# Kernel optimization log

Hardware: AMD Instinct MI355X
Metric: run time of the kernel (lower is better)

## Reference

```python
import jax, jax.numpy as jnp
import numpy as np

N_NODES = 50000
N_EDGES = 320000
D_IN = 256
D_OUT = 256


def setup_inputs() -> dict:
    key = jax.random.key(0)
    k1, k2, k3, k4, k5, k6, k7 = jax.random.split(key, 7)
    s = 1.0 / np.sqrt(D_IN)
    return {
        "node_features": jax.random.normal(k1, (N_NODES, D_IN), dtype=jnp.float32),
        "edge_index": jax.random.randint(k2, (2, N_EDGES), 0, N_NODES, dtype=jnp.int64),
        "w1": jax.random.uniform(k3, (D_OUT, D_IN), jnp.float32, -s, s),
        "w2": jax.random.uniform(k4, (D_OUT, D_IN), jnp.float32, -s, s),
        "w3": jax.random.uniform(k5, (D_OUT, D_IN), jnp.float32, -s, s),
        "b3": jax.random.uniform(k6, (D_OUT,), jnp.float32, -s, s),
    }


def reference(node_features, edge_index, w1, w2, w3, b3):
    # GraphSAGE-style conv: project, gather messages from senders,
    # scatter-sum at receivers, project, combine with self term.
    n = node_features.shape[0]
    proj = node_features @ w3.T + b3                 # [N, D_OUT]
    msgs = proj[edge_index[0]]                       # [E, D_OUT] gather senders
    agg = jax.ops.segment_sum(msgs, edge_index[1], num_segments=n)  # [N, D_OUT]
    out = node_features @ w1.T + agg @ w2.T          # [N, D_OUT]
    return out
```

## Files before the change

kernel.cpp:

```cpp
#include <hip/hip_runtime.h>

#define NN 50000
#define NPAD 50048
#define NE 320000
#define D 256
#define CAP 64

typedef __bf16 bf16x8 __attribute__((ext_vector_type(8)));
typedef float f32x4 __attribute__((ext_vector_type(4)));

__device__ __forceinline__ unsigned short f2bf(float f) {
    unsigned u = __builtin_bit_cast(unsigned, f);
    unsigned r = u + 0x7FFFu + ((u >> 16) & 1u);
    return (unsigned short)(r >> 16);
}
__device__ __forceinline__ float bf2f(unsigned short h) {
    return __builtin_bit_cast(float, (unsigned)h << 16);
}

__global__ __launch_bounds__(256) void prep_weights(
        const float* __restrict__ w1, const float* __restrict__ w2,
        const float* __restrict__ w3, const float* __restrict__ b3,
        unsigned short* __restrict__ WTT, float* __restrict__ bvec) {
    const int j = blockIdx.x;
    const int k = threadIdx.x;
    __shared__ float w2row[D];
    __shared__ float red[D];
    w2row[k] = w2[j * D + k];
    __syncthreads();
    float acc = 0.f;
    #pragma unroll 8
    for (int o = 0; o < D; ++o) acc += w2row[o] * w3[o * D + k];
    WTT[(size_t)j * 512 + k]       = f2bf(w1[j * D + k]);
    WTT[(size_t)j * 512 + D + k]   = f2bf(acc);
    red[k] = w2row[k] * b3[k];
    __syncthreads();
    for (int s = 128; s > 0; s >>= 1) {
        if (k < s) red[k] += red[k + s];
        __syncthreads();
    }
    if (k == 0) bvec[j] = red[0];
}

__global__ __launch_bounds__(256) void convert_x(
        const float* __restrict__ x, unsigned short* __restrict__ xbf) {
    const size_t i = ((size_t)blockIdx.x * 256 + threadIdx.x) * 8;
    if (i >= (size_t)NN * D) return;
    const float4 a = *reinterpret_cast<const float4*>(x + i);
    const float4 b = *reinterpret_cast<const float4*>(x + i + 4);
    ushort4 o0 = {f2bf(a.x), f2bf(a.y), f2bf(a.z), f2bf(a.w)};
    ushort4 o1 = {f2bf(b.x), f2bf(b.y), f2bf(b.z), f2bf(b.w)};
    *reinterpret_cast<ushort4*>(xbf + i)     = o0;
    *reinterpret_cast<ushort4*>(xbf + i + 4) = o1;
}

__global__ __launch_bounds__(256) void fill_csr(
        const int* __restrict__ ei, int* __restrict__ csr, int* __restrict__ cnt) {
    const int e = blockIdx.x * 256 + threadIdx.x;
    if (e >= NE) return;
    const int src = ei[e];
    const int dst = ei[NE + e];
    const int pos = atomicAdd(cnt + dst, 1);
    if (pos < CAP) csr[(size_t)dst * CAP + pos] = src;
}

__global__ __launch_bounds__(256) void agg_gather(
        const unsigned short* __restrict__ xbf, const int* __restrict__ csr,
        const int* __restrict__ cnt, unsigned short* __restrict__ aggbf) {
    const int node = blockIdx.x * 4 + (threadIdx.x >> 6);
    const int lane = threadIdx.x & 63;
    if (node >= NN) return;
    int d = cnt[node]; if (d > CAP) d = CAP;
    const int* __restrict__ row = csr + (size_t)node * CAP;
    float a0 = 0.f, a1 = 0.f, a2 = 0.f, a3 = 0.f;
    int i = 0;
    for (; i + 2 <= d; i += 2) {
        const ushort4 v0 = *reinterpret_cast<const ushort4*>(xbf + (size_t)row[i] * D + lane * 4);
        const ushort4 v1 = *reinterpret_cast<const ushort4*>(xbf + (size_t)row[i + 1] * D + lane * 4);
        a0 += bf2f(v0.x) + bf2f(v1.x); a1 += bf2f(v0.y) + bf2f(v1.y);
        a2 += bf2f(v0.z) + bf2f(v1.z); a3 += bf2f(v0.w) + bf2f(v1.w);
    }
    if (i < d) {
        const ushort4 v = *reinterpret_cast<const ushort4*>(xbf + (size_t)row[i] * D + lane * 4);
        a0 += bf2f(v.x); a1 += bf2f(v.y); a2 += bf2f(v.z); a3 += bf2f(v.w);
    }
    ushort4 o = {f2bf(a0), f2bf(a1), f2bf(a2), f2bf(a3)};
    *reinterpret_cast<ushort4*>(aggbf + (size_t)node * D + lane * 4) = o;
}

__global__ __launch_bounds__(256) void gemm_mfma(
        const unsigned short* __restrict__ xbf, const unsigned short* __restrict__ aggbf,
        const unsigned short* __restrict__ WTT, const float* __restrict__ bvec,
        const int* __restrict__ cnt, float* __restrict__ out) {
    __shared__ __align__(16) unsigned short ldsA[128 * 64];
    __shared__ __align__(16) unsigned short ldsB[128 * 64];

    const int tid  = threadIdx.x;
    const int w    = tid >> 6;
    const int lane = tid & 63;
    const int wm   = w >> 1, wn = w & 1;
    const int mb   = blockIdx.x >> 1;
    const int nb0  = (blockIdx.x & 1) * 128;
    const int gr0  = mb * 128;

    f32x4 acc[4][4];
    #pragma unroll
    for (int a = 0; a < 4; ++a)
        #pragma unroll
        for (int b = 0; b < 4; ++b) acc[a][b] = (f32x4)0.f;

    for (int kt = 0; kt < 8; ++kt) {
        if (kt) __syncthreads();
        {
            const unsigned short* __restrict__ src = (kt < 4) ? xbf : aggbf;
            const int kc = (kt & 3) * 64;
            #pragma unroll
            for (int p = 0; p < 4; ++p) {
                const int idx = p * 256 + w * 64 + lane;
                const int r = idx >> 3, c = idx & 7;
                const int gcol = kc + ((c ^ (r & 7)) << 3);
                const unsigned short* gp = src + ((size_t)(gr0 + r) << 8) + gcol;
                unsigned short* lp = &ldsA[(size_t)(p * 256 + w * 64) << 3];
                __builtin_amdgcn_global_load_lds(
                    (const __attribute__((address_space(1))) void*)(const void*)gp,
                    (__attribute__((address_space(3))) void*)(void*)lp, 16, 0, 0);
            }
        }
        {
            const int kc = kt * 64;
            #pragma unroll
            for (int p = 0; p < 4; ++p) {
                const int idx = p * 256 + w * 64 + lane;
                const int r = idx >> 3, c = idx & 7;
                const int gcol = kc + ((c ^ (r & 7)) << 3);
                const unsigned short* gp = WTT + ((size_t)(nb0 + r) << 9) + gcol;
                unsigned short* lp = &ldsB[(size_t)(p * 256 + w * 64) << 3];
                __builtin_amdgcn_global_load_lds(
                    (const __attribute__((address_space(1))) void*)(const void*)gp,
                    (__attribute__((address_space(3))) void*)(void*)lp, 16, 0, 0);
            }
        }
        __syncthreads();

        #pragma unroll
        for (int kh = 0; kh < 2; ++kh) {
            const int cbase = kh * 4 + (lane >> 4);
            bf16x8 af[4], bf[4];
            #pragma unroll
            for (int f = 0; f < 4; ++f) {
                const int ra = wm * 64 + f * 16 + (lane & 15);
                af[f] = *reinterpret_cast<const bf16x8*>(
                    &ldsA[ra * 64 + ((cbase ^ (ra & 7)) << 3)]);
                const int rb = wn * 64 + f * 16 + (lane & 15);
                bf[f] = *reinterpret_cast<const bf16x8*>(
                    &ldsB[rb * 64 + ((cbase ^ (rb & 7)) << 3)]);
            }
            #pragma unroll
            for (int fm = 0; fm < 4; ++fm)
                #pragma unroll
                for (int fn = 0; fn < 4; ++fn)
                    acc[fm][fn] = __builtin_amdgcn_mfma_f32_16x16x32_bf16(
                        af[fm], bf[fn], acc[fm][fn], 0, 0, 0);
        }
    }

    const int col0 = nb0 + wn * 64 + (lane & 15);
    float bv[4];
    #pragma unroll
    for (int fn = 0; fn < 4; ++fn) bv[fn] = bvec[col0 + fn * 16];
    #pragma unroll
    for (int fm = 0; fm < 4; ++fm) {
        #pragma unroll
        for (int i = 0; i < 4; ++i) {
            const int row = gr0 + wm * 64 + fm * 16 + ((lane >> 4) << 2) + i;
            if (row < NN) {
                const float dg = (float)cnt[row];
                float* op = out + ((size_t)row << 8) + col0;
                #pragma unroll
                for (int fn = 0; fn < 4; ++fn)
                    op[fn * 16] = acc[fm][fn][i] + dg * bv[fn];
            }
        }
    }
}

extern "C" void kernel_launch(void* const* d_in, const int* in_sizes, int n_in,
                              void* d_out, int out_size, void* d_ws, size_t ws_size,
                              hipStream_t stream) {
    const float* x  = (const float*)d_in[0];
    const int*   ei = (const int*)d_in[1];
    const float* w1 = (const float*)d_in[2];
    const float* w2 = (const float*)d_in[3];
    const float* w3 = (const float*)d_in[4];
    const float* b3 = (const float*)d_in[5];
    float* out = (float*)d_out;

    unsigned short* xbf   = (unsigned short*)d_ws;
    unsigned short* aggbf = xbf + (size_t)NPAD * D;
    unsigned short* WTT   = aggbf + (size_t)NPAD * D;
    float* bvec = (float*)(WTT + (size_t)D * 512);
    int*   cnt  = (int*)(bvec + D);
    int*   csr  = cnt + NN;

    hipMemsetAsync(cnt, 0, NN * sizeof(int), stream);
    prep_weights<<<D, 256, 0, stream>>>(w1, w2, w3, b3, WTT, bvec);
    convert_x<<<(NN * D) / (256 * 8), 256, 0, stream>>>(x, xbf);
    fill_csr<<<(NE + 255) / 256, 256, 0, stream>>>(ei, csr, cnt);
    agg_gather<<<(NN + 3) / 4, 256, 0, stream>>>(xbf, csr, cnt, aggbf);
    gemm_mfma<<<((NN + 127) / 128) * 2, 256, 0, stream>>>(xbf, aggbf, WTT, bvec, cnt, out);
}
```

Measured before the change: 113.3 us.

## Double-buffer GEMM LDS tiles and fold count zeroing into convert kernel

The GEMM kernel now keeps two LDS buffers for the A and B tiles. It issues the global-to-LDS loads for the next K step before computing on the current one, so memory latency overlaps with MFMA work, and it needs only one barrier per iteration. Separately, the hipMemsetAsync that zeroed the degree counts is removed and the zeroing moves into convert_x, which saves one launch. The double buffer doubles LDS use per block to 64KB, which may lower occupancy. It also relies on the next barrier to make the asynchronous LDS loads visible.

```diff
diff --git a/kernel.cpp b/kernel.cpp
--- a/kernel.cpp
+++ b/kernel.cpp
@@ -43,8 +43,11 @@
 }
 
 __global__ __launch_bounds__(256) void convert_x(
-        const float* __restrict__ x, unsigned short* __restrict__ xbf) {
-    const size_t i = ((size_t)blockIdx.x * 256 + threadIdx.x) * 8;
+        const float* __restrict__ x, unsigned short* __restrict__ xbf,
+        int* __restrict__ cnt) {
+    const size_t gid = (size_t)blockIdx.x * 256 + threadIdx.x;
+    if (gid < NN) cnt[gid] = 0;
+    const size_t i = gid * 8;
     if (i >= (size_t)NN * D) return;
     const float4 a = *reinterpret_cast<const float4*>(x + i);
     const float4 b = *reinterpret_cast<const float4*>(x + i + 4);
@@ -92,8 +95,8 @@
         const unsigned short* __restrict__ xbf, const unsigned short* __restrict__ aggbf,
         const unsigned short* __restrict__ WTT, const float* __restrict__ bvec,
         const int* __restrict__ cnt, float* __restrict__ out) {
-    __shared__ __align__(16) unsigned short ldsA[128 * 64];
-    __shared__ __align__(16) unsigned short ldsB[128 * 64];
+    __shared__ __align__(16) unsigned short ldsA[2][128 * 64];
+    __shared__ __align__(16) unsigned short ldsB[2][128 * 64];
 
     const int tid  = threadIdx.x;
     const int w    = tid >> 6;
@@ -103,65 +106,61 @@
     const int nb0  = (blockIdx.x & 1) * 128;
     const int gr0  = mb * 128;
 
+    auto stage = [&](int kt, int b) {
+        const unsigned short* __restrict__ srcA = (kt < 4) ? xbf : aggbf;
+        const int kcA = (kt & 3) * 64;
+        const int kcB = kt * 64;
+        #pragma unroll
+        for (int p = 0; p < 4; ++p) {
+            const int idx = p * 256 + w * 64 + lane;
+            const int r = idx >> 3, c = idx & 7;
+            const int sw = (c ^ (r & 7)) << 3;
+            const unsigned short* gpA = srcA + ((size_t)(gr0 + r) << 8) + kcA + sw;
+            unsigned short* lpA = &ldsA[b][(p * 256 + w * 64) << 3];
+            __builtin_amdgcn_global_load_lds(
+                (const __attribute__((address_space(1))) void*)(const void*)gpA,
+                (__attribute__((address_space(3))) void*)(void*)lpA, 16, 0, 0);
+            const unsigned short* gpB = WTT + ((size_t)(nb0 + r) << 9) + kcB + sw;
+            unsigned short* lpB = &ldsB[b][(p * 256 + w * 64) << 3];
+            __builtin_amdgcn_global_load_lds(
+                (const __attribute__((address_space(1))) void*)(const void*)gpB,
+                (__attribute__((address_space(3))) void*)(void*)lpB, 16, 0, 0);
+        }
+    };
+
     f32x4 acc[4][4];
     #pragma unroll
     for (int a = 0; a < 4; ++a)
         #pragma unroll
         for (int b = 0; b < 4; ++b) acc[a][b] = (f32x4)0.f;
 
+    stage(0, 0);
+    __syncthreads();
+    #pragma unroll 2
     for (int kt = 0; kt < 8; ++kt) {
-        if (kt) __syncthreads();
-        {
-            const unsigned short* __restrict__ src = (kt < 4) ? xbf : aggbf;
-            const int kc = (kt & 3) * 64;
-            #pragma unroll
-            for (int p = 0; p < 4; ++p) {
-                const int idx = p * 256 + w * 64 + lane;
-                const int r = idx >> 3, c = idx & 7;
-                const int gcol = kc + ((c ^ (r & 7)) << 3);
-                const unsigned short* gp = src + ((size_t)(gr0 + r) << 8) + gcol;
-                unsigned short* lp = &ldsA[(size_t)(p * 256 + w * 64) << 3];
-                __builtin_amdgcn_global_load_lds(
-                    (const __attribute__((address_space(1))) void*)(const void*)gp,
-                    (__attribute__((address_space(3))) void*)(void*)lp, 16, 0, 0);
-            }
-        }
-        {
-            const int kc = kt * 64;
-            #pragma unroll
-            for (int p = 0; p < 4; ++p) {
-                const int idx = p * 256 + w * 64 + lane;
-                const int r = idx >> 3, c = idx & 7;
-                const int gcol = kc + ((c ^ (r & 7)) << 3);
-                const unsigned short* gp = WTT + ((size_t)(nb0 + r) << 9) + gcol;
-                unsigned short* lp = &ldsB[(size_t)(p * 256 + w * 64) << 3];
-                __builtin_amdgcn_global_load_lds(
-                    (const __attribute__((address_space(1))) void*)(const void*)gp,
-                    (__attribute__((address_space(3))) void*)(void*)lp, 16, 0, 0);
-            }
-        }
-        __syncthreads();
-
+        const int cur = kt & 1;
+        if (kt < 7) stage(kt + 1, cur ^ 1);
         #pragma unroll
         for (int kh = 0; kh < 2; ++kh) {
             const int cbase = kh * 4 + (lane >> 4);
-            bf16x8 af[4], bf[4];
+            bf16x8 af[4], bfr[4];
             #pragma unroll
             for (int f = 0; f < 4; ++f) {
                 const int ra = wm * 64 + f * 16 + (lane & 15);
                 af[f] = *reinterpret_cast<const bf16x8*>(
-                    &ldsA[ra * 64 + ((cbase ^ (ra & 7)) << 3)]);
+                    &ldsA[cur][ra * 64 + ((cbase ^ (ra & 7)) << 3)]);
                 const int rb = wn * 64 + f * 16 + (lane & 15);
-                bf[f] = *reinterpret_cast<const bf16x8*>(
-                    &ldsB[rb * 64 + ((cbase ^ (rb & 7)) << 3)]);
+                bfr[f] = *reinterpret_cast<const bf16x8*>(
+                    &ldsB[cur][rb * 64 + ((cbase ^ (rb & 7)) << 3)]);
             }
             #pragma unroll
             for (int fm = 0; fm < 4; ++fm)
                 #pragma unroll
                 for (int fn = 0; fn < 4; ++fn)
                     acc[fm][fn] = __builtin_amdgcn_mfma_f32_16x16x32_bf16(
-                        af[fm], bf[fn], acc[fm][fn], 0, 0, 0);
+                        af[fm], bfr[fn], acc[fm][fn], 0, 0, 0);
         }
+        __syncthreads();
     }
 
     const int col0 = nb0 + wn * 64 + (lane & 15);
@@ -202,9 +201,8 @@
     int*   cnt  = (int*)(bvec + D);
     int*   csr  = cnt + NN;
 
-    hipMemsetAsync(cnt, 0, NN * sizeof(int), stream);
     prep_weights<<<D, 256, 0, stream>>>(w1, w2, w3, b3, WTT, bvec);
-    convert_x<<<(NN * D) / (256 * 8), 256, 0, stream>>>(x, xbf);
+    convert_x<<<(NN * D) / (256 * 8), 256, 0, stream>>>(x, xbf, cnt);
     fill_csr<<<(NE + 255) / 256, 256, 0, stream>>>(ei, csr, cnt);
     agg_gather<<<(NN + 3) / 4, 256, 0, stream>>>(xbf, csr, cnt, aggbf);
     gemm_mfma<<<((NN + 127) / 128) * 2, 256, 0, stream>>>(xbf, aggbf, WTT, bvec, cnt, out);
```

Result: no change. 112.0 us (-1.2%).
